# Kernel optimization log

Measured on AMD Instinct MI355X. Metric: run time of the kernel, lower is better.

## Reference

```python
import jax, jax.numpy as jnp
import numpy as np

ATTN_DIM = 64

def setup_inputs() -> dict:
    key = jax.random.key(0)
    k1, k2, k3, k4, k5 = jax.random.split(key, 5)
    B, S, E, D = 4, 2048, 16, 256
    return {
        "input_gate": jax.random.uniform(k1, (B, S, E, 1), dtype=jnp.float32),
        "q_expert_vector": jax.random.normal(k2, (B, S, E, D), dtype=jnp.float32),
        "k_expert_vector": jax.random.normal(k3, (B, S, E, D), dtype=jnp.float32),
        "Wq": jax.random.normal(k4, (D, ATTN_DIM), dtype=jnp.float32) * 0.02,
        "Wk": jax.random.normal(k5, (D, ATTN_DIM), dtype=jnp.float32) * 0.02,
    }

def reference(input_gate, q_expert_vector, k_expert_vector, Wq, Wk):
    # project: (B,S,E,D) @ (D,A) -> (B,S,E,A)
    query = jnp.einsum("bsed,da->bsea", q_expert_vector, Wq)
    key = jnp.einsum("bsed,da->bsea", k_expert_vector, Wk)
    # attention over experts: (B,S,E,E)
    sim = jnp.einsum("bsqa,bska->bsqk", query, key) / jnp.sqrt(
        jnp.asarray(ATTN_DIM, dtype=query.dtype))
    sim = jax.nn.softmax(sim, axis=-1)
    # gate: (B,S,E,E) @ (B,S,E,1) -> (B,S,E,1)
    gate = jnp.matmul(sim, input_gate)
    routing_weight = jax.nn.softmax(gate.squeeze(-1), axis=-1)  # (B,S,E)
    return routing_weight
```

## Files before the change

kernel.cpp:

```cpp
#include <hip/hip_runtime.h>
#include <hip/hip_bf16.h>

typedef __attribute__((ext_vector_type(8))) short short8;
typedef __attribute__((ext_vector_type(4))) float f32x4;

#define WPB 16
#define BLOCK 1024
#define TPW 2
#define W_PITCH 528
#define W_MAT (64 * W_PITCH)
#define QK_PITCH 144
#define QK_TILE (16 * QK_PITCH)
#define LDS_W (2 * W_MAT)
#define SCR_PW (2 * QK_TILE)
#define LDS_TOTAL (LDS_W + WPB * SCR_PW)

union S8U { short8 s; unsigned u[4]; };

__device__ __forceinline__ unsigned pk2(float a, float b) {
  __hip_bfloat162 h = __float22bfloat162_rn(make_float2(a, b));
  return *reinterpret_cast<unsigned*>(&h);
}
__device__ __forceinline__ unsigned short bf1(float a) {
  __hip_bfloat16 h = __float2bfloat16(a);
  return *reinterpret_cast<unsigned short*>(&h);
}

#define PROJF(XROW, WLDS, ACC) {                                              \
  float4 xb_[16];                                                             \
  _Pragma("unroll") for (int i = 0; i < 16; ++i)                              \
    xb_[i] = *(const float4*)((XROW) + (i >> 1) * 32 + (i & 1) * 4);          \
  _Pragma("unroll") for (int ks = 0; ks < 8; ++ks) {                          \
    S8U u_;                                                                   \
    u_.u[0] = pk2(xb_[2 * ks].x, xb_[2 * ks].y);                              \
    u_.u[1] = pk2(xb_[2 * ks].z, xb_[2 * ks].w);                              \
    u_.u[2] = pk2(xb_[2 * ks + 1].x, xb_[2 * ks + 1].y);                      \
    u_.u[3] = pk2(xb_[2 * ks + 1].z, xb_[2 * ks + 1].w);                      \
    short8 af_ = u_.s;                                                        \
    _Pragma("unroll") for (int n = 0; n < 4; ++n) {                           \
      short8 bf_ = *(const short8*)((WLDS) + (n * 16 + e) * W_PITCH + ks * 64 + g * 16); \
      ACC[n] = __builtin_amdgcn_mfma_f32_16x16x32_bf16(af_, bf_, ACC[n], 0, 0, 0); \
    }                                                                         \
  } }

#define WRITET(ACC, TB) {                                                     \
  unsigned short* tw_ = (unsigned short*)(TB);                                \
  _Pragma("unroll") for (int n = 0; n < 4; ++n)                               \
    _Pragma("unroll") for (int r = 0; r < 4; ++r)                             \
      tw_[(g * 4 + r) * 72 + n * 16 + e] = bf1(ACC[n][r]); }

__global__ __launch_bounds__(BLOCK) void attrouter_kernel(
    const float* __restrict__ ig, const float* __restrict__ qev,
    const float* __restrict__ kev, const float* __restrict__ Wq,
    const float* __restrict__ Wk, float* __restrict__ out, int ntok)
{
  extern __shared__ char smem[];
  const int tid  = threadIdx.x;
  const int lane = tid & 63;
  const int wv   = tid >> 6;
  const int e    = lane & 15;
  const int g    = lane >> 4;

  {
    #pragma unroll
    for (int i = 0; i < 2; ++i) {
      int tile = tid + i * BLOCK;
      int m  = tile >> 10;
      int r  = tile & 1023;
      int d0 = (r >> 4) * 4;
      int a0 = (r & 15) * 4;
      const float* wsrc = m ? Wk : Wq;
      const float scl = m ? 1.0f : 0.125f;
      const float* src = wsrc + d0 * 64 + a0;
      float4 r0 = *(const float4*)(src);
      float4 r1 = *(const float4*)(src + 64);
      float4 r2 = *(const float4*)(src + 128);
      float4 r3 = *(const float4*)(src + 192);
      float c0[4] = {r0.x, r0.y, r0.z, r0.w};
      float c1[4] = {r1.x, r1.y, r1.z, r1.w};
      float c2[4] = {r2.x, r2.y, r2.z, r2.w};
      float c3[4] = {r3.x, r3.y, r3.z, r3.w};
      #pragma unroll
      for (int j = 0; j < 4; ++j) {
        uint2 v;
        v.x = pk2(scl * c0[j], scl * c1[j]);
        v.y = pk2(scl * c2[j], scl * c3[j]);
        *(uint2*)(smem + m * W_MAT + (a0 + j) * W_PITCH + d0 * 2) = v;
      }
    }
  }
  __syncthreads();

  char* qt = smem + LDS_W + wv * SCR_PW;
  char* kt = qt + QK_TILE;

  const int wbase = (blockIdx.x * WPB + wv) * TPW;

  #pragma unroll
  for (int t = 0; t < TPW; ++t) {
    const int tok = wbase + t;
    if (tok >= ntok) break;
    const float* qrow = qev + (size_t)tok * 4096 + e * 256 + g * 8;
    const float* krow = kev + (size_t)tok * 4096 + e * 256 + g * 8;

    f32x4 aq[4] = {{0,0,0,0},{0,0,0,0},{0,0,0,0},{0,0,0,0}};
    PROJF(qrow, smem, aq);
    WRITET(aq, qt);

    f32x4 ak[4] = {{0,0,0,0},{0,0,0,0},{0,0,0,0},{0,0,0,0}};
    PROJF(krow, smem + W_MAT, ak);
    WRITET(ak, kt);

    short8 fq0 = *(const short8*)(qt + e * QK_PITCH + g * 16);
    short8 fq1 = *(const short8*)(qt + e * QK_PITCH + 64 + g * 16);
    short8 fk0 = *(const short8*)(kt + e * QK_PITCH + g * 16);
    short8 fk1 = *(const short8*)(kt + e * QK_PITCH + 64 + g * 16);
    f32x4 s = {0, 0, 0, 0};
    s = __builtin_amdgcn_mfma_f32_16x16x32_bf16(fk0, fq0, s, 0, 0, 0);
    s = __builtin_amdgcn_mfma_f32_16x16x32_bf16(fk1, fq1, s, 0, 0, 0);

    float4 igv = *(const float4*)(ig + (size_t)tok * 16 + g * 4);
    float p0 = __expf(s[0]), p1 = __expf(s[1]);
    float p2 = __expf(s[2]), p3 = __expf(s[3]);
    float sg = p0 * igv.x + p1 * igv.y + p2 * igv.z + p3 * igv.w;
    float se = (p0 + p1) + (p2 + p3);
    sg += __shfl_xor(sg, 16); se += __shfl_xor(se, 16);
    sg += __shfl_xor(sg, 32); se += __shfl_xor(se, 32);
    float ev = __expf(sg / se);
    float ss = ev;
    ss += __shfl_xor(ss, 1); ss += __shfl_xor(ss, 2);
    ss += __shfl_xor(ss, 4); ss += __shfl_xor(ss, 8);
    if (g == 0) out[(size_t)tok * 16 + e] = ev / ss;
  }
}

extern "C" void kernel_launch(void* const* d_in, const int* in_sizes, int n_in,
                              void* d_out, int out_size, void* d_ws, size_t ws_size,
                              hipStream_t stream) {
  const float* ig  = (const float*)d_in[0];
  const float* qev = (const float*)d_in[1];
  const float* kev = (const float*)d_in[2];
  const float* Wq  = (const float*)d_in[3];
  const float* Wk  = (const float*)d_in[4];
  float* out = (float*)d_out;
  int ntok = in_sizes[1] >> 12;

  hipFuncSetAttribute((const void*)attrouter_kernel,
                      hipFuncAttributeMaxDynamicSharedMemorySize, LDS_TOTAL);

  int grid = (ntok + WPB * TPW - 1) / (WPB * TPW);
  attrouter_kernel<<<grid, BLOCK, LDS_TOTAL, stream>>>(ig, qev, kev, Wq, Wk, out, ntok);
}
```

Before: 50.06 us.

## Stage token inputs through LDS with prefetch and split projection across waves

Each block now handles 32 tokens over 8 iterations. Four waves cooperate per token: q versus k, and two halves of the output columns. Inputs are loaded with coalesced float4 reads, converted to bf16 and staged in LDS, while the next iteration's data is prefetched into registers during the current MFMA compute. The aim is to improve global load coalescing and overlap memory latency with compute. In exchange it adds block-wide barriers each iteration and leaves most waves idle during the small attention and softmax phase.

```diff
diff --git a/kernel.cpp b/kernel.cpp
--- a/kernel.cpp
+++ b/kernel.cpp
@@ -4,18 +4,20 @@
 typedef __attribute__((ext_vector_type(8))) short short8;
 typedef __attribute__((ext_vector_type(4))) float f32x4;
 
-#define WPB 16
 #define BLOCK 1024
-#define TPW 2
+#define TPI 4
+#define NIT 8
+#define TPB (TPI * NIT)
 #define W_PITCH 528
 #define W_MAT (64 * W_PITCH)
-#define QK_PITCH 144
-#define QK_TILE (16 * QK_PITCH)
 #define LDS_W (2 * W_MAT)
-#define SCR_PW (2 * QK_TILE)
-#define LDS_TOTAL (LDS_W + WPB * SCR_PW)
-
-union S8U { short8 s; unsigned u[4]; };
+#define X_PITCH 528
+#define X_BLK (16 * X_PITCH)
+#define XB LDS_W
+#define LDS_X (TPI * 2 * X_BLK)
+#define CB (XB + LDS_X)
+#define C_PAIR 4608
+#define LDS_TOTAL (CB + TPI * C_PAIR)
 
 __device__ __forceinline__ unsigned pk2(float a, float b) {
   __hip_bfloat162 h = __float22bfloat162_rn(make_float2(a, b));
@@ -25,29 +27,6 @@
   __hip_bfloat16 h = __float2bfloat16(a);
   return *reinterpret_cast<unsigned short*>(&h);
 }
-
-#define PROJF(XROW, WLDS, ACC) {                                              \
-  float4 xb_[16];                                                             \
-  _Pragma("unroll") for (int i = 0; i < 16; ++i)                              \
-    xb_[i] = *(const float4*)((XROW) + (i >> 1) * 32 + (i & 1) * 4);          \
-  _Pragma("unroll") for (int ks = 0; ks < 8; ++ks) {                          \
-    S8U u_;                                                                   \
-    u_.u[0] = pk2(xb_[2 * ks].x, xb_[2 * ks].y);                              \
-    u_.u[1] = pk2(xb_[2 * ks].z, xb_[2 * ks].w);                              \
-    u_.u[2] = pk2(xb_[2 * ks + 1].x, xb_[2 * ks + 1].y);                      \
-    u_.u[3] = pk2(xb_[2 * ks + 1].z, xb_[2 * ks + 1].w);                      \
-    short8 af_ = u_.s;                                                        \
-    _Pragma("unroll") for (int n = 0; n < 4; ++n) {                           \
-      short8 bf_ = *(const short8*)((WLDS) + (n * 16 + e) * W_PITCH + ks * 64 + g * 16); \
-      ACC[n] = __builtin_amdgcn_mfma_f32_16x16x32_bf16(af_, bf_, ACC[n], 0, 0, 0); \
-    }                                                                         \
-  } }
-
-#define WRITET(ACC, TB) {                                                     \
-  unsigned short* tw_ = (unsigned short*)(TB);                                \
-  _Pragma("unroll") for (int n = 0; n < 4; ++n)                               \
-    _Pragma("unroll") for (int r = 0; r < 4; ++r)                             \
-      tw_[(g * 4 + r) * 72 + n * 16 + e] = bf1(ACC[n][r]); }
 
 __global__ __launch_bounds__(BLOCK) void attrouter_kernel(
     const float* __restrict__ ig, const float* __restrict__ qev,
@@ -91,46 +70,86 @@
   }
   __syncthreads();
 
-  char* qt = smem + LDS_W + wv * SCR_PW;
-  char* kt = qt + QK_TILE;
+  const int t4  = wv >> 2;
+  const int tns = (wv >> 1) & 1;
+  const int hn  = wv & 1;
 
-  const int wbase = (blockIdx.x * WPB + wv) * TPW;
+  const float* xsrc = tns ? kev : qev;
+  char* xdst = smem + XB + (t4 * 2 + tns) * X_BLK + hn * 8 * X_PITCH + lane * 8;
+  const char* xcomp = smem + XB + (t4 * 2 + tns) * X_BLK;
+  const char* wlds  = smem + tns * W_MAT;
+  unsigned short* ctile = (unsigned short*)(smem + CB + t4 * C_PAIR + tns * 2304);
+  const int n0 = hn * 2, n1 = n0 + 1;
 
-  #pragma unroll
-  for (int t = 0; t < TPW; ++t) {
-    const int tok = wbase + t;
-    if (tok >= ntok) break;
-    const float* qrow = qev + (size_t)tok * 4096 + e * 256 + g * 8;
-    const float* krow = kev + (size_t)tok * 4096 + e * 256 + g * 8;
+  const int tb0 = blockIdx.x * TPB;
+  float4 xb[8];
 
-    f32x4 aq[4] = {{0,0,0,0},{0,0,0,0},{0,0,0,0},{0,0,0,0}};
-    PROJF(qrow, smem, aq);
-    WRITET(aq, qt);
+#define LOADIT(IT) {                                                          \
+    int tok_ = tb0 + (IT) * TPI + t4; if (tok_ >= ntok) tok_ = ntok - 1;      \
+    const float* p_ = xsrc + (size_t)tok_ * 4096 + hn * 2048 + lane * 4;      \
+    _Pragma("unroll") for (int r = 0; r < 8; ++r)                             \
+      xb[r] = *(const float4*)(p_ + r * 256); }
 
-    f32x4 ak[4] = {{0,0,0,0},{0,0,0,0},{0,0,0,0},{0,0,0,0}};
-    PROJF(krow, smem + W_MAT, ak);
-    WRITET(ak, kt);
+#define STAGEW() {                                                            \
+    _Pragma("unroll") for (int r = 0; r < 8; ++r) {                           \
+      uint2 v_; v_.x = pk2(xb[r].x, xb[r].y); v_.y = pk2(xb[r].z, xb[r].w);   \
+      *(uint2*)(xdst + r * X_PITCH) = v_; } }
 
-    short8 fq0 = *(const short8*)(qt + e * QK_PITCH + g * 16);
-    short8 fq1 = *(const short8*)(qt + e * QK_PITCH + 64 + g * 16);
-    short8 fk0 = *(const short8*)(kt + e * QK_PITCH + g * 16);
-    short8 fk1 = *(const short8*)(kt + e * QK_PITCH + 64 + g * 16);
-    f32x4 s = {0, 0, 0, 0};
-    s = __builtin_amdgcn_mfma_f32_16x16x32_bf16(fk0, fq0, s, 0, 0, 0);
-    s = __builtin_amdgcn_mfma_f32_16x16x32_bf16(fk1, fq1, s, 0, 0, 0);
+  LOADIT(0);
+  __builtin_amdgcn_sched_barrier(0);
+  STAGEW();
+  __syncthreads();
 
-    float4 igv = *(const float4*)(ig + (size_t)tok * 16 + g * 4);
-    float p0 = __expf(s[0]), p1 = __expf(s[1]);
-    float p2 = __expf(s[2]), p3 = __expf(s[3]);
-    float sg = p0 * igv.x + p1 * igv.y + p2 * igv.z + p3 * igv.w;
-    float se = (p0 + p1) + (p2 + p3);
-    sg += __shfl_xor(sg, 16); se += __shfl_xor(se, 16);
-    sg += __shfl_xor(sg, 32); se += __shfl_xor(se, 32);
-    float ev = __expf(sg / se);
-    float ss = ev;
-    ss += __shfl_xor(ss, 1); ss += __shfl_xor(ss, 2);
-    ss += __shfl_xor(ss, 4); ss += __shfl_xor(ss, 8);
-    if (g == 0) out[(size_t)tok * 16 + e] = ev / ss;
+  for (int it = 0; it < NIT; ++it) {
+    const bool pf = (it + 1 < NIT);
+    if (pf) LOADIT(it + 1);
+    __builtin_amdgcn_sched_barrier(0);
+
+    f32x4 a0 = {0,0,0,0}, a1 = {0,0,0,0};
+    #pragma unroll
+    for (int ks = 0; ks < 8; ++ks) {
+      short8 af = *(const short8*)(xcomp + e * X_PITCH + ks * 64 + g * 16);
+      short8 b0 = *(const short8*)(wlds + (n0 * 16 + e) * W_PITCH + ks * 64 + g * 16);
+      short8 b1 = *(const short8*)(wlds + (n1 * 16 + e) * W_PITCH + ks * 64 + g * 16);
+      a0 = __builtin_amdgcn_mfma_f32_16x16x32_bf16(af, b0, a0, 0, 0, 0);
+      a1 = __builtin_amdgcn_mfma_f32_16x16x32_bf16(af, b1, a1, 0, 0, 0);
+    }
+    #pragma unroll
+    for (int r = 0; r < 4; ++r) {
+      ctile[(g * 4 + r) * 72 + n0 * 16 + e] = bf1(a0[r]);
+      ctile[(g * 4 + r) * 72 + n1 * 16 + e] = bf1(a1[r]);
+    }
+    __syncthreads();
+
+    if (pf) STAGEW();
+
+    if (wv < TPI) {
+      const int tok = tb0 + it * TPI + wv;
+      if (tok < ntok) {
+        const char* qt = smem + CB + wv * C_PAIR;
+        const char* kt = qt + 2304;
+        short8 fq0 = *(const short8*)(qt + e * 144 + g * 16);
+        short8 fq1 = *(const short8*)(qt + e * 144 + 64 + g * 16);
+        short8 fk0 = *(const short8*)(kt + e * 144 + g * 16);
+        short8 fk1 = *(const short8*)(kt + e * 144 + 64 + g * 16);
+        f32x4 s = {0,0,0,0};
+        s = __builtin_amdgcn_mfma_f32_16x16x32_bf16(fk0, fq0, s, 0, 0, 0);
+        s = __builtin_amdgcn_mfma_f32_16x16x32_bf16(fk1, fq1, s, 0, 0, 0);
+        float4 igv = *(const float4*)(ig + (size_t)tok * 16 + g * 4);
+        float p0 = __expf(s[0]), p1 = __expf(s[1]);
+        float p2 = __expf(s[2]), p3 = __expf(s[3]);
+        float sg = p0 * igv.x + p1 * igv.y + p2 * igv.z + p3 * igv.w;
+        float se = (p0 + p1) + (p2 + p3);
+        sg += __shfl_xor(sg, 16); se += __shfl_xor(se, 16);
+        sg += __shfl_xor(sg, 32); se += __shfl_xor(se, 32);
+        float ev = __expf(sg / se);
+        float ss = ev;
+        ss += __shfl_xor(ss, 1); ss += __shfl_xor(ss, 2);
+        ss += __shfl_xor(ss, 4); ss += __shfl_xor(ss, 8);
+        if (g == 0) out[(size_t)tok * 16 + e] = ev / ss;
+      }
+    }
+    __syncthreads();
   }
 }
 
@@ -148,6 +167,6 @@
   hipFuncSetAttribute((const void*)attrouter_kernel,
                       hipFuncAttributeMaxDynamicSharedMemorySize, LDS_TOTAL);
 
-  int grid = (ntok + WPB * TPW - 1) / (WPB * TPW);
+  int grid = (ntok + TPB - 1) / TPB;
   attrouter_kernel<<<grid, BLOCK, LDS_TOTAL, stream>>>(ig, qev, kev, Wq, Wk, out, ntok);
 }
```

New measurement: 49.60 us. Within noise of the previous version (-0.9%).

## Software-pipeline global row loads across q/k projections with sched barriers

Applied to the files above, without the earlier changes.

Restructures the per-wave loop into a pipeline over four rows (q and k for each of two tokens). Each row's 256-float input is loaded in two halves, and the next half or row is issued before the MFMA work on the current one, with sched_barrier keeping the compiler from reordering. The goal is to hide global memory latency behind matrix math in this bandwidth-heavy kernel. Out-of-range tokens are clamped to a valid index instead of breaking early, and only the store is guarded. This raises register pressure from the raw and converted buffers.

```diff
diff --git a/kernel.cpp b/kernel.cpp
--- a/kernel.cpp
+++ b/kernel.cpp
@@ -7,6 +7,7 @@
 #define WPB 16
 #define BLOCK 1024
 #define TPW 2
+#define NROW (2 * TPW)
 #define W_PITCH 528
 #define W_MAT (64 * W_PITCH)
 #define QK_PITCH 144
@@ -26,28 +27,36 @@
   return *reinterpret_cast<unsigned short*>(&h);
 }
 
-#define PROJF(XROW, WLDS, ACC) {                                              \
-  float4 xb_[16];                                                             \
-  _Pragma("unroll") for (int i = 0; i < 16; ++i)                              \
-    xb_[i] = *(const float4*)((XROW) + (i >> 1) * 32 + (i & 1) * 4);          \
-  _Pragma("unroll") for (int ks = 0; ks < 8; ++ks) {                          \
+#define ISSUE(RP, H) {                                                        \
+  _Pragma("unroll") for (int j_ = 0; j_ < 4; ++j_) {                          \
+    raw[2 * j_]     = *(const float4*)((RP) + (4 * (H) + j_) * 32);           \
+    raw[2 * j_ + 1] = *(const float4*)((RP) + (4 * (H) + j_) * 32 + 4);       \
+  } }
+
+#define CONV(H) {                                                             \
+  _Pragma("unroll") for (int j_ = 0; j_ < 4; ++j_) {                          \
     S8U u_;                                                                   \
-    u_.u[0] = pk2(xb_[2 * ks].x, xb_[2 * ks].y);                              \
-    u_.u[1] = pk2(xb_[2 * ks].z, xb_[2 * ks].w);                              \
-    u_.u[2] = pk2(xb_[2 * ks + 1].x, xb_[2 * ks + 1].y);                      \
-    u_.u[3] = pk2(xb_[2 * ks + 1].z, xb_[2 * ks + 1].w);                      \
-    short8 af_ = u_.s;                                                        \
-    _Pragma("unroll") for (int n = 0; n < 4; ++n) {                           \
-      short8 bf_ = *(const short8*)((WLDS) + (n * 16 + e) * W_PITCH + ks * 64 + g * 16); \
-      ACC[n] = __builtin_amdgcn_mfma_f32_16x16x32_bf16(af_, bf_, ACC[n], 0, 0, 0); \
-    }                                                                         \
+    u_.u[0] = pk2(raw[2 * j_].x, raw[2 * j_].y);                              \
+    u_.u[1] = pk2(raw[2 * j_].z, raw[2 * j_].w);                              \
+    u_.u[2] = pk2(raw[2 * j_ + 1].x, raw[2 * j_ + 1].y);                      \
+    u_.u[3] = pk2(raw[2 * j_ + 1].z, raw[2 * j_ + 1].w);                      \
+    bfb[4 * (H) + j_] = u_.s;                                                 \
   } }
+
+#define MF(K0, WL, ACC) {                                                     \
+  _Pragma("unroll") for (int ks_ = (K0); ks_ < (K0) + 4; ++ks_) {             \
+    _Pragma("unroll") for (int n_ = 0; n_ < 4; ++n_) {                        \
+      short8 b_ = *(const short8*)((WL) + (n_ * 16 + e) * W_PITCH + ks_ * 64 + g * 16); \
+      ACC[n_] = __builtin_amdgcn_mfma_f32_16x16x32_bf16(bfb[ks_], b_, ACC[n_], 0, 0, 0); \
+    } }  }
 
 #define WRITET(ACC, TB) {                                                     \
   unsigned short* tw_ = (unsigned short*)(TB);                                \
-  _Pragma("unroll") for (int n = 0; n < 4; ++n)                               \
-    _Pragma("unroll") for (int r = 0; r < 4; ++r)                             \
-      tw_[(g * 4 + r) * 72 + n * 16 + e] = bf1(ACC[n][r]); }
+  _Pragma("unroll") for (int n_ = 0; n_ < 4; ++n_)                            \
+    _Pragma("unroll") for (int r_ = 0; r_ < 4; ++r_)                          \
+      tw_[(g * 4 + r_) * 72 + n_ * 16 + e] = bf1(ACC[n_][r_]); }
+
+#define SBAR __builtin_amdgcn_sched_barrier(0)
 
 __global__ __launch_bounds__(BLOCK) void attrouter_kernel(
     const float* __restrict__ ig, const float* __restrict__ qev,
@@ -93,44 +102,58 @@
 
   char* qt = smem + LDS_W + wv * SCR_PW;
   char* kt = qt + QK_TILE;
-
   const int wbase = (blockIdx.x * WPB + wv) * TPW;
 
+  const float* rp[NROW];
+  int tkn[TPW];
   #pragma unroll
   for (int t = 0; t < TPW; ++t) {
-    const int tok = wbase + t;
-    if (tok >= ntok) break;
-    const float* qrow = qev + (size_t)tok * 4096 + e * 256 + g * 8;
-    const float* krow = kev + (size_t)tok * 4096 + e * 256 + g * 8;
+    tkn[t] = (wbase + t < ntok) ? (wbase + t) : (ntok - 1);
+    rp[2 * t]     = qev + (size_t)tkn[t] * 4096 + e * 256 + g * 8;
+    rp[2 * t + 1] = kev + (size_t)tkn[t] * 4096 + e * 256 + g * 8;
+  }
 
-    f32x4 aq[4] = {{0,0,0,0},{0,0,0,0},{0,0,0,0},{0,0,0,0}};
-    PROJF(qrow, smem, aq);
-    WRITET(aq, qt);
+  float4 raw[8];
+  short8 bfb[8];
 
-    f32x4 ak[4] = {{0,0,0,0},{0,0,0,0},{0,0,0,0},{0,0,0,0}};
-    PROJF(krow, smem + W_MAT, ak);
-    WRITET(ak, kt);
+  ISSUE(rp[0], 0); SBAR;
 
-    short8 fq0 = *(const short8*)(qt + e * QK_PITCH + g * 16);
-    short8 fq1 = *(const short8*)(qt + e * QK_PITCH + 64 + g * 16);
-    short8 fk0 = *(const short8*)(kt + e * QK_PITCH + g * 16);
-    short8 fk1 = *(const short8*)(kt + e * QK_PITCH + 64 + g * 16);
-    f32x4 s = {0, 0, 0, 0};
-    s = __builtin_amdgcn_mfma_f32_16x16x32_bf16(fk0, fq0, s, 0, 0, 0);
-    s = __builtin_amdgcn_mfma_f32_16x16x32_bf16(fk1, fq1, s, 0, 0, 0);
+  #pragma unroll
+  for (int r = 0; r < NROW; ++r) {
+    const char* wl = smem + (r & 1) * W_MAT;
+    f32x4 acc[4] = {{0,0,0,0},{0,0,0,0},{0,0,0,0},{0,0,0,0}};
 
-    float4 igv = *(const float4*)(ig + (size_t)tok * 16 + g * 4);
-    float p0 = __expf(s[0]), p1 = __expf(s[1]);
-    float p2 = __expf(s[2]), p3 = __expf(s[3]);
-    float sg = p0 * igv.x + p1 * igv.y + p2 * igv.z + p3 * igv.w;
-    float se = (p0 + p1) + (p2 + p3);
-    sg += __shfl_xor(sg, 16); se += __shfl_xor(se, 16);
-    sg += __shfl_xor(sg, 32); se += __shfl_xor(se, 32);
-    float ev = __expf(sg / se);
-    float ss = ev;
-    ss += __shfl_xor(ss, 1); ss += __shfl_xor(ss, 2);
-    ss += __shfl_xor(ss, 4); ss += __shfl_xor(ss, 8);
-    if (g == 0) out[(size_t)tok * 16 + e] = ev / ss;
+    CONV(0);
+    ISSUE(rp[r], 1); SBAR;
+    MF(0, wl, acc);
+    CONV(1);
+    if (r < NROW - 1) { ISSUE(rp[r + 1], 0); SBAR; }
+    MF(4, wl, acc);
+    WRITET(acc, (r & 1) ? kt : qt);
+
+    if (r & 1) {
+      const int tok = tkn[r >> 1];
+      short8 fq0 = *(const short8*)(qt + e * QK_PITCH + g * 16);
+      short8 fq1 = *(const short8*)(qt + e * QK_PITCH + 64 + g * 16);
+      short8 fk0 = *(const short8*)(kt + e * QK_PITCH + g * 16);
+      short8 fk1 = *(const short8*)(kt + e * QK_PITCH + 64 + g * 16);
+      f32x4 s = {0,0,0,0};
+      s = __builtin_amdgcn_mfma_f32_16x16x32_bf16(fk0, fq0, s, 0, 0, 0);
+      s = __builtin_amdgcn_mfma_f32_16x16x32_bf16(fk1, fq1, s, 0, 0, 0);
+      float4 igv = *(const float4*)(ig + (size_t)tok * 16 + g * 4);
+      float p0 = __expf(s[0]), p1 = __expf(s[1]);
+      float p2 = __expf(s[2]), p3 = __expf(s[3]);
+      float sg = p0 * igv.x + p1 * igv.y + p2 * igv.z + p3 * igv.w;
+      float se = (p0 + p1) + (p2 + p3);
+      sg += __shfl_xor(sg, 16); se += __shfl_xor(se, 16);
+      sg += __shfl_xor(sg, 32); se += __shfl_xor(se, 32);
+      float ev = __expf(sg / se);
+      float ss = ev;
+      ss += __shfl_xor(ss, 1); ss += __shfl_xor(ss, 2);
+      ss += __shfl_xor(ss, 4); ss += __shfl_xor(ss, 8);
+      if (g == 0 && wbase + (r >> 1) < ntok)
+        out[(size_t)tok * 16 + e] = ev / ss;
+    }
   }
 }
 
```

Result: no change. 50.55 us (+1.0%).
